# Kernel tuning notes

Hardware: AMD Instinct MI355X
Metric: run time of the kernel (lower is better)

Reference implementation:

```python
import jax, jax.numpy as jnp
import numpy as np

B, SEQ, PRED, ENC = 32, 720, 96, 321
LAYERS, SCALE = 2, 2
SEG = [48, 24]
D = [512, 256]
SNX = [SEQ // s for s in SEG]   # [15, 30]
SNY = [PRED // s for s in SEG]  # [2, 4]


def _gru(x, h, Wih, Whh, bih, bhh):
    # torch.nn.GRUCell math
    gi = x @ Wih.T + bih
    gh = h @ Whh.T + bhh
    i_r, i_z, i_n = jnp.split(gi, 3, axis=-1)
    h_r, h_z, h_n = jnp.split(gh, 3, axis=-1)
    r = jax.nn.sigmoid(i_r + h_r)
    z = jax.nn.sigmoid(i_z + h_z)
    n = jnp.tanh(i_n + r * h_n)
    return (1.0 - z) * n + z * h


def setup_inputs():
    key = jax.random.key(0)
    ks = iter(jax.random.split(key, 40))
    inp = {"x": jax.random.normal(next(ks), (B, SEQ, ENC), jnp.float32)}
    sc = 0.02
    for i in range(LAYERS):
        d, s = D[i], SEG[i]
        inp[f"W_emb{i}"] = jax.random.normal(next(ks), (d, s), jnp.float32) * sc
        inp[f"b_emb{i}"] = jnp.zeros((d,), jnp.float32)
        inp[f"Wih{i}"] = jax.random.normal(next(ks), (3 * d, d), jnp.float32) * sc
        inp[f"Whh{i}"] = jax.random.normal(next(ks), (3 * d, d), jnp.float32) * sc
        inp[f"bih{i}"] = jnp.zeros((3 * d,), jnp.float32)
        inp[f"bhh{i}"] = jnp.zeros((3 * d,), jnp.float32)
        inp[f"Wpred{i}"] = jax.random.normal(next(ks), (s, d), jnp.float32) * sc
        inp[f"bpred{i}"] = jnp.zeros((s,), jnp.float32)
        inp[f"pos{i}"] = jax.random.normal(next(ks), (SNY[i], d // 2), jnp.float32)
        inp[f"chan{i}"] = jax.random.normal(next(ks), (ENC, d // 2), jnp.float32)
    return inp


def _forward(x, params):
    seq_last = jax.lax.stop_gradient(x[:, -1:, :])   # [B,1,ENC] (detached in torch)
    xc = (x - seq_last).transpose(0, 2, 1)            # [B,ENC,SEQ]
    out = jnp.zeros((B, PRED, ENC), x.dtype)
    for i in range(LAYERS):
        p = params[i]
        d, s, T, S = D[i], SEG[i], SNX[i], SNY[i]
        # value embedding: [B*ENC, T, seg_len] -> [B*ENC, T, d]
        xe = jax.nn.relu(jnp.einsum('nts,ds->ntd', xc.reshape(-1, T, s), p['W_emb']) + p['b_emb'])
        if i == 0:
            seq = xe.transpose(1, 0, 2)   # all seg_num_x[0] segments in order
        else:
            # faithful to source: finer layer always consumes segments 0..scale^(i+1)-1
            # once per outer step, seg_num_x[0] times in total
            k = SCALE ** (i + 1)
            idx = np.tile(np.arange(k), SNX[0])
            seq = xe[:, idx].transpose(1, 0, 2)
        h0 = jnp.zeros((xe.shape[0], d), x.dtype)
        step = lambda h, xt: (_gru(xt, h, p['Wih'], p['Whh'], p['bih'], p['bhh']), None)
        h_fin, _ = jax.lax.scan(step, h0, seq)   # [B*ENC, d]
        # decoder: seg_num_y independent GRU cell applications (no carried state)
        half = d // 2
        pos = jnp.concatenate([
            jnp.broadcast_to(p['pos'][None], (ENC, S, half)),
            jnp.broadcast_to(p['chan'][:, None], (ENC, S, half))], axis=-1).reshape(ENC * S, d)
        pos = jnp.tile(pos, (B, 1)).reshape(S, B * ENC, d)   # contiguous chunks per step
        hn = jnp.repeat(h_fin, S, axis=0).reshape(S, B * ENC, d)
        hy = _gru(pos, hn, p['Wih'], p['Whh'], p['bih'], p['bhh'])   # [S, B*ENC, d]
        y = hy.reshape(S * B * ENC, d) @ p['Wpred'].T + p['bpred']   # [S*B*ENC, seg_len]
        y = y.reshape(-1, ENC, PRED).transpose(0, 2, 1)              # [B, PRED, ENC]
        out = out + y + seq_last
    return out / LAYERS


def reference(x, W_emb0, b_emb0, Wih0, Whh0, bih0, bhh0, Wpred0, bpred0, pos0, chan0,
              W_emb1, b_emb1, Wih1, Whh1, bih1, bhh1, Wpred1, bpred1, pos1, chan1):
    params = [
        dict(W_emb=W_emb0, b_emb=b_emb0, Wih=Wih0, Whh=Whh0, bih=bih0, bhh=bhh0,
             Wpred=Wpred0, bpred=bpred0, pos=pos0, chan=chan0),
        dict(W_emb=W_emb1, b_emb=b_emb1, Wih=Wih1, Whh=Whh1, bih=bih1, bhh=bhh1,
             Wpred=Wpred1, bpred=bpred1, pos=pos1, chan=chan1),
    ]
    return _forward(x, params)
```

## Files before the change

### kernel.cpp

```cpp
#include <hip/hip_runtime.h>
#include <math.h>


#define NB     10272
#define MP     10368
#define ENC_   321
#define SEQ_   720
#define PRED_  96
#define BATCH_ 32

typedef long long i64;
typedef unsigned short u16;
typedef unsigned int u32;
using bf16x8 = __attribute__((ext_vector_type(8))) short;
using f32x4  = __attribute__((ext_vector_type(4))) float;
using u16x4  = __attribute__((ext_vector_type(4))) unsigned short;

#define AS1 __attribute__((address_space(1)))
#define AS3 __attribute__((address_space(3)))
#define GLOAD16(g, l) __builtin_amdgcn_global_load_lds((const AS1 void*)(g), (AS3 void*)(l), 16, 0, 0)
#define MFMA16(a, b, c) __builtin_amdgcn_mfma_f32_16x16x32_bf16(a, b, c, 0, 0, 0)

__device__ __forceinline__ float bf2f(u16 u) {
    union { u32 i; float f; } v; v.i = ((u32)u) << 16; return v.f;
}
__device__ __forceinline__ u16 f2bf(float f) {
    union { float f; u32 i; } v; v.f = f;
    return (u16)((v.i + 0x7fff + ((v.i >> 16) & 1)) >> 16);
}
__device__ __forceinline__ float sigf(float x) {
    x = fminf(fmaxf(x, -30.f), 30.f);
    return 1.f / (1.f + __expf(-x));
}
__device__ __forceinline__ float tanhfast(float x) {
    x = fminf(fmaxf(x, -15.f), 15.f);
    float e = __expf(2.f * x);
    return (e - 1.f) / (e + 1.f);
}
__device__ __forceinline__ void swz(int idx, int NXT, int NYT, int& mt, int& nt) {
    int per = NYT * 8;
    int grp = idx / per;
    int base = grp * 8;
    int mg = NXT - base; if (mg > 8) mg = 8;
    int rem = idx - grp * per;
    mt = base + rem % mg;
    nt = rem / mg;
}

__global__ __launch_bounds__(256) void zero_bf(u16* __restrict__ b, i64 n) {
    i64 i = (i64)blockIdx.x * 256 + threadIdx.x;
    i64 n2 = n >> 1;
    if (i < n2) ((u32*)b)[i] = 0;
}

__global__ __launch_bounds__(256) void convert_pad(const float* __restrict__ src,
                                                   u16* __restrict__ dst,
                                                   int R, int C, int Rp, int Cp) {
    i64 idx = (i64)blockIdx.x * 256 + threadIdx.x;
    i64 total = (i64)Rp * Cp;
    if (idx >= total) return;
    int r = (int)(idx / Cp);
    int c = (int)(idx - (i64)r * Cp);
    dst[idx] = (r < R && c < C) ? f2bf(src[(i64)r * C + c]) : (u16)0;
}

__global__ __launch_bounds__(256) void seg_gather_bf(const float* __restrict__ x,
                                                     u16* __restrict__ dst,
                                                     int t0, int T, int s, int Kp) {
    i64 idx = (i64)blockIdx.x * 256 + threadIdx.x;
    i64 per_t = (i64)MP * Kp;
    i64 total = (i64)T * per_t;
    if (idx >= total) return;
    int t = (int)(idx / per_t);
    i64 rem = idx - (i64)t * per_t;
    int j = (int)(rem / MP);
    int n = (int)(rem - (i64)j * MP);
    float v = 0.f;
    if (n < NB && j < s) {
        int b = n / ENC_, e = n - b * ENC_;
        const float* xb = x + (i64)b * SEQ_ * ENC_ + e;
        v = xb[(i64)((t0 + t) * s + j) * ENC_] - xb[(i64)(SEQ_ - 1) * ENC_];
    }
    dst[((i64)t * MP + n) * Kp + j] = f2bf(v);
}

__global__ __launch_bounds__(256) void pmat_fill_bf(const float* __restrict__ pos,
                                                    const float* __restrict__ chan,
                                                    u16* __restrict__ dst,
                                                    int S, int d, int Rp) {
    i64 idx = (i64)blockIdx.x * 256 + threadIdx.x;
    i64 total = (i64)Rp * d;
    if (idx >= total) return;
    int row = (int)(idx / d);
    int c = (int)(idx - (i64)row * d);
    float v = 0.f;
    if (row < ENC_ * S) {
        int e = row / S, sy = row - e * S;
        int half = d >> 1;
        v = (c < half) ? pos[sy * half + c] : chan[e * half + (c - half)];
    }
    dst[idx] = f2bf(v);
}

__global__ __launch_bounds__(256) void out_kernel(const float* __restrict__ x,
                                                  const float* __restrict__ y0,
                                                  const float* __restrict__ y1,
                                                  float* __restrict__ out) {
    int idx = blockIdx.x * 256 + threadIdx.x;
    const int total = BATCH_ * PRED_ * ENC_;
    if (idx >= total) return;
    int b = idx / (PRED_ * ENC_);
    int r = idx - b * (PRED_ * ENC_);
    int p = r / ENC_;
    int e = r - p * ENC_;
    int n = b * ENC_ + e;
    float sl = x[(i64)b * SEQ_ * ENC_ + (i64)(SEQ_ - 1) * ENC_ + e];
    out[idx] = sl + 0.5f * (y0[(i64)n * PRED_ + p] + y1[(i64)n * PRED_ + p]);
}

template<int MODE>
__global__ __launch_bounds__(256) void gemm_bf16mfma(const u16* __restrict__ A,
                                                     const u16* __restrict__ B,
                                                     const float* __restrict__ bias,
                                                     void* __restrict__ Cp,
                                                     int K, int Mstore, int Nstore,
                                                     int ldc, int NXT, int NYT) {
    __shared__ u16 smA[128 * 64];
    __shared__ u16 smB[128 * 64];
    const int tid = threadIdx.x;
    const int w = tid >> 6, l = tid & 63;
    int mt, nt; swz(blockIdx.x, NXT, NYT, mt, nt);
    const int m0 = mt * 128, n0 = nt * 128;
    const int srow = (l >> 3) & 7, pch = l & 7;
    const int cch = pch ^ srow;
    const u16* ga[4]; const u16* gb[4];
#pragma unroll
    for (int r = 0; r < 4; ++r) {
        int seg = r * 4 + w;
        ga[r] = A + (i64)(m0 + seg * 8 + srow) * K + cch * 8;
        gb[r] = B + (i64)(n0 + seg * 8 + srow) * K + cch * 8;
    }
    f32x4 acc[4][4] = {};
    const int lr = l & 15, lg = l >> 4;
    const int wm = (w >> 1) * 64, wn = (w & 1) * 64;
    for (int kk = 0; kk < K; kk += 64) {
#pragma unroll
        for (int r = 0; r < 4; ++r) { GLOAD16(ga[r], smA + (r * 4 + w) * 512); ga[r] += 64; }
#pragma unroll
        for (int r = 0; r < 4; ++r) { GLOAD16(gb[r], smB + (r * 4 + w) * 512); gb[r] += 64; }
        __syncthreads();
#pragma unroll
        for (int s = 0; s < 2; ++s) {
            const int ph = ((s * 4 + lg) ^ (lr & 7)) * 8;
            bf16x8 av[4], bv[4];
#pragma unroll
            for (int i = 0; i < 4; ++i)
                av[i] = *(const bf16x8*)(smA + (wm + i * 16 + lr) * 64 + ph);
#pragma unroll
            for (int j = 0; j < 4; ++j)
                bv[j] = *(const bf16x8*)(smB + (wn + j * 16 + lr) * 64 + ph);
#pragma unroll
            for (int i = 0; i < 4; ++i)
#pragma unroll
                for (int j = 0; j < 4; ++j)
                    acc[i][j] = MFMA16(av[i], bv[j], acc[i][j]);
        }
        __syncthreads();
    }
    if (MODE == 3) {
        const int NCTG = ldc >> 4;
#pragma unroll
        for (int i = 0; i < 4; ++i) {
            int mt16 = (m0 + wm + i * 16) >> 4;
#pragma unroll
            for (int j = 0; j < 4; ++j) {
                int cb = n0 + wn + j * 16;
                if (cb >= Nstore) continue;
                float bs = bias[cb + lr];
                u16x4 sv;
#pragma unroll
                for (int r = 0; r < 4; ++r) sv[r] = f2bf(acc[i][j][r] + bs);
                *(u16x4*)((u16*)Cp + ((i64)mt16 * NCTG + (cb >> 4)) * 256 + l * 4) = sv;
            }
        }
        return;
    }
#pragma unroll
    for (int i = 0; i < 4; ++i) {
        int mbase = m0 + wm + i * 16 + 4 * lg;
#pragma unroll
        for (int j = 0; j < 4; ++j) {
            int c = n0 + wn + j * 16 + lr;
            if (c >= Nstore) continue;
            float bs = bias[c];
#pragma unroll
            for (int r = 0; r < 4; ++r) {
                int mm = mbase + r;
                if (mm < Mstore) {
                    float v = acc[i][j][r] + bs;
                    if (MODE == 2) v = fmaxf(v, 0.f);
                    if (MODE == 0) ((float*)Cp)[(i64)mm * ldc + c] = v;
                    else           ((u16*)Cp)[(i64)mm * ldc + c] = f2bf(v);
                }
            }
        }
    }
}

template<int D>
__global__ __launch_bounds__(256, 3) void gru_step(const u16* __restrict__ xe,
                                                   const u16* __restrict__ hsrc,
                                                   const u16* __restrict__ Wih,
                                                   const u16* __restrict__ Whh,
                                                   const float* __restrict__ bih,
                                                   const float* __restrict__ bhh,
                                                   u16* __restrict__ hdst) {
    __shared__ u16 smA[64 * 64];
    __shared__ u16 smB[3 * 64 * 64];
    __shared__ u16 smH[64 * 64];
    const int tid = threadIdx.x;
    const int w = tid >> 6, l = tid & 63;
    const int m0 = blockIdx.x * 64;
    const int c0 = blockIdx.y * 64;
    const int srow = (l >> 3) & 7, pch = l & 7;
    const int cch = pch ^ srow;
    const int lr = l & 15, lg = l >> 4;
    f32x4 aR[4] = {}, aZ[4] = {}, aNI[4] = {}, aNH[4] = {};
#pragma unroll
    for (int phase = 0; phase < 2; ++phase) {
        const u16* Abase = phase ? hsrc : xe;
        const u16* Bbase = phase ? Whh : Wih;
        const u16* ga[2]; const u16* gb[6];
#pragma unroll
        for (int r = 0; r < 2; ++r)
            ga[r] = Abase + (i64)(m0 + (r * 4 + w) * 8 + srow) * D + cch * 8;
#pragma unroll
        for (int q = 0; q < 6; ++q) {
            int gs = q * 4 + w;
            int g = gs >> 3, sp = gs & 7;
            gb[q] = Bbase + (i64)(g * D + c0 + sp * 8 + srow) * D + cch * 8;
        }
        for (int kk = 0; kk < D; kk += 64) {
#pragma unroll
            for (int r = 0; r < 2; ++r) GLOAD16(ga[r], smA + (r * 4 + w) * 512);
            if (phase == 1 && kk == c0) {
#pragma unroll
                for (int r = 0; r < 2; ++r) GLOAD16(ga[r], smH + (r * 4 + w) * 512);
            }
#pragma unroll
            for (int r = 0; r < 2; ++r) ga[r] += 64;
#pragma unroll
            for (int q = 0; q < 6; ++q) { GLOAD16(gb[q], smB + (q * 4 + w) * 512); gb[q] += 64; }
            __syncthreads();
#pragma unroll
            for (int s = 0; s < 2; ++s) {
                const int phs = ((s * 4 + lg) ^ (lr & 7)) * 8;
                bf16x8 av = *(const bf16x8*)(smA + (w * 16 + lr) * 64 + phs);
#pragma unroll
                for (int j = 0; j < 4; ++j) {
                    bf16x8 b0 = *(const bf16x8*)(smB + 0 * 4096 + (j * 16 + lr) * 64 + phs);
                    bf16x8 b1 = *(const bf16x8*)(smB + 1 * 4096 + (j * 16 + lr) * 64 + phs);
                    bf16x8 b2 = *(const bf16x8*)(smB + 2 * 4096 + (j * 16 + lr) * 64 + phs);
                    aR[j] = MFMA16(av, b0, aR[j]);
                    aZ[j] = MFMA16(av, b1, aZ[j]);
                    if (phase == 0)
                        aNI[j] = MFMA16(av, b2, aNI[j]);
                    else
                        aNH[j] = MFMA16(av, b2, aNH[j]);
                }
            }
            __syncthreads();
        }
    }
    const int rowb = m0 + w * 16 + 4 * lg;
#pragma unroll
    for (int j = 0; j < 4; ++j) {
        const int cc = c0 + j * 16 + lr;
        float bR = bih[cc] + bhh[cc];
        float bZ = bih[D + cc] + bhh[D + cc];
        float bNI = bih[2 * D + cc];
        float bNH = bhh[2 * D + cc];
#pragma unroll
        for (int r = 0; r < 4; ++r) {
            const int lrow = w * 16 + 4 * lg + r;
            const int lcol = j * 16 + lr;
            float ho = bf2f(smH[lrow * 64 + ((((lcol >> 3)) ^ (lrow & 7)) << 3) + (lcol & 7)]);
            float rr = sigf(aR[j][r] + bR);
            float zz = sigf(aZ[j][r] + bZ);
            float nn = tanhfast(aNI[j][r] + bNI + rr * (aNH[j][r] + bNH));
            hdst[(i64)(rowb + r) * D + cc] = f2bf((1.f - zz) * nn + zz * ho);
        }
    }
}

template<int D>
__global__ __launch_bounds__(256, 3) void gru_step_h(const u16* __restrict__ gi,
                                                     const u16* __restrict__ hsrc,
                                                     const u16* __restrict__ Whh,
                                                     const float* __restrict__ bhh,
                                                     u16* __restrict__ hdst) {
    constexpr int NCT = D / 16;
    constexpr int NCTG = 3 * D / 16;
    __shared__ u16 smA[64 * 64];
    __shared__ u16 smB[3 * 64 * 64];
    __shared__ u16 smH[64 * 64];
    const int tid = threadIdx.x;
    const int w = tid >> 6, l = tid & 63;
    const int m0 = blockIdx.x * 64;
    const int c0 = blockIdx.y * 64;
    const int srow = (l >> 3) & 7, pch = l & 7;
    const int cch = pch ^ srow;
    const int lr = l & 15, lg = l >> 4;
    f32x4 aR[4] = {}, aZ[4] = {}, aNH[4] = {};
    const u16* ga[2]; const u16* gb[6];
#pragma unroll
    for (int r = 0; r < 2; ++r)
        ga[r] = hsrc + (i64)(m0 + (r * 4 + w) * 8 + srow) * D + cch * 8;
#pragma unroll
    for (int q = 0; q < 6; ++q) {
        int gs = q * 4 + w;
        int g = gs >> 3, sp = gs & 7;
        gb[q] = Whh + (i64)(g * D + c0 + sp * 8 + srow) * D + cch * 8;
    }
    const int Trow = (m0 >> 4) + w;
    const i64 gbase = (i64)Trow * NCTG * 256 + l * 4;
    u16x4 g0[4], g1[4], g2[4];
    for (int kk = 0; kk < D; kk += 64) {
#pragma unroll
        for (int r = 0; r < 2; ++r) GLOAD16(ga[r], smA + (r * 4 + w) * 512);
        if (kk == c0) {
#pragma unroll
            for (int r = 0; r < 2; ++r) GLOAD16(ga[r], smH + (r * 4 + w) * 512);
        }
#pragma unroll
        for (int r = 0; r < 2; ++r) ga[r] += 64;
#pragma unroll
        for (int q = 0; q < 6; ++q) { GLOAD16(gb[q], smB + (q * 4 + w) * 512); gb[q] += 64; }
        __syncthreads();
        if (kk == D - 64) {
#pragma unroll
            for (int j = 0; j < 4; ++j) {
                const int ct = (c0 >> 4) + j;
                g0[j] = *(const u16x4*)(gi + gbase + (i64)(0 * NCT + ct) * 256);
                g1[j] = *(const u16x4*)(gi + gbase + (i64)(1 * NCT + ct) * 256);
                g2[j] = *(const u16x4*)(gi + gbase + (i64)(2 * NCT + ct) * 256);
            }
        }
#pragma unroll
        for (int s = 0; s < 2; ++s) {
            const int phs = ((s * 4 + lg) ^ (lr & 7)) * 8;
            bf16x8 av = *(const bf16x8*)(smA + (w * 16 + lr) * 64 + phs);
#pragma unroll
            for (int j = 0; j < 4; ++j) {
                bf16x8 b0 = *(const bf16x8*)(smB + 0 * 4096 + (j * 16 + lr) * 64 + phs);
                bf16x8 b1 = *(const bf16x8*)(smB + 1 * 4096 + (j * 16 + lr) * 64 + phs);
                bf16x8 b2 = *(const bf16x8*)(smB + 2 * 4096 + (j * 16 + lr) * 64 + phs);
                aR[j] = MFMA16(av, b0, aR[j]);
                aZ[j] = MFMA16(av, b1, aZ[j]);
                aNH[j] = MFMA16(av, b2, aNH[j]);
            }
        }
        __syncthreads();
    }
    const int rowb = m0 + w * 16 + 4 * lg;
#pragma unroll
    for (int j = 0; j < 4; ++j) {
        const int cc = c0 + j * 16 + lr;
        float bR = bhh[cc];
        float bZ = bhh[D + cc];
        float bNH = bhh[2 * D + cc];
#pragma unroll
        for (int r = 0; r < 4; ++r) {
            const int lrow = w * 16 + 4 * lg + r;
            const int lcol = j * 16 + lr;
            float ho = bf2f(smH[lrow * 64 + ((((lcol >> 3)) ^ (lrow & 7)) << 3) + (lcol & 7)]);
            float rr = sigf(bf2f(g0[j][r]) + aR[j][r] + bR);
            float zz = sigf(bf2f(g1[j][r]) + aZ[j][r] + bZ);
            float nn = tanhfast(bf2f(g2[j][r]) + rr * (aNH[j][r] + bNH));
            hdst[(i64)(rowb + r) * D + cc] = f2bf((1.f - zz) * nn + zz * ho);
        }
    }
}

template<int D, int S>
__global__ __launch_bounds__(256) void gru_dec(const u16* __restrict__ Asrc,
                                               const u16* __restrict__ Whh,
                                               const float* __restrict__ bhh,
                                               const u16* __restrict__ gi,
                                               u16* __restrict__ hy) {
    constexpr int NYT = D / 64;
    __shared__ u16 smA[128 * 64];
    __shared__ u16 smB[3 * 64 * 64];
    const int tid = threadIdx.x;
    const int w = tid >> 6, l = tid & 63;
    int mt, nt; swz(blockIdx.x, 81, NYT, mt, nt);
    const int m0 = mt * 128;
    const int c0 = nt * 64;
    const int srow = (l >> 3) & 7, pch = l & 7;
    const int cch = pch ^ srow;
    const u16* ga[4]; const u16* gb[6];
#pragma unroll
    for (int r = 0; r < 4; ++r)
        ga[r] = Asrc + (i64)(m0 + (r * 4 + w) * 8 + srow) * D + cch * 8;
#pragma unroll
    for (int q = 0; q < 6; ++q) {
        int gs = q * 4 + w;
        int g = gs >> 3, sp = gs & 7;
        gb[q] = Whh + (i64)(g * D + c0 + sp * 8 + srow) * D + cch * 8;
    }
    f32x4 acc[3][4][2] = {};
    const int lr = l & 15, lg = l >> 4;
    const int wm = (w >> 1) * 64, wc = (w & 1) * 32;
    for (int kk = 0; kk < D; kk += 64) {
#pragma unroll
        for (int r = 0; r < 4; ++r) { GLOAD16(ga[r], smA + (r * 4 + w) * 512); ga[r] += 64; }
#pragma unroll
        for (int q = 0; q < 6; ++q) { GLOAD16(gb[q], smB + (q * 4 + w) * 512); gb[q] += 64; }
        __syncthreads();
#pragma unroll
        for (int s = 0; s < 2; ++s) {
            const int ph = ((s * 4 + lg) ^ (lr & 7)) * 8;
            bf16x8 av[4], bv[3][2];
#pragma unroll
            for (int i = 0; i < 4; ++i)
                av[i] = *(const bf16x8*)(smA + (wm + i * 16 + lr) * 64 + ph);
#pragma unroll
            for (int g = 0; g < 3; ++g)
#pragma unroll
                for (int j = 0; j < 2; ++j)
                    bv[g][j] = *(const bf16x8*)(smB + g * 4096 + (wc + j * 16 + lr) * 64 + ph);
#pragma unroll
            for (int g = 0; g < 3; ++g)
#pragma unroll
                for (int i = 0; i < 4; ++i)
#pragma unroll
                    for (int j = 0; j < 2; ++j)
                        acc[g][i][j] = MFMA16(av[i], bv[g][j], acc[g][i][j]);
        }
        __syncthreads();
    }
#pragma unroll
    for (int i = 0; i < 4; ++i) {
        const int rowb = m0 + wm + 16 * i + 4 * lg;
        int e0 = rowb % ENC_;
#pragma unroll
        for (int j = 0; j < 2; ++j) {
            const int cc = c0 + wc + 16 * j + lr;
            float b0 = bhh[cc], b1 = bhh[D + cc], b2 = bhh[2 * D + cc];
#pragma unroll
            for (int r = 0; r < 4; ++r) {
                int mm = rowb + r;
                if (mm >= NB) continue;
                int e = e0 + r; if (e >= ENC_) e -= ENC_;
                float ho = bf2f(Asrc[(i64)mm * D + cc]);
                float hr = acc[0][i][j][r] + b0;
                float hz = acc[1][i][j][r] + b1;
                float hn2 = acc[2][i][j][r] + b2;
#pragma unroll
                for (int sy = 0; sy < S; ++sy) {
                    i64 gib = (i64)(e * S + sy) * 3 * D + cc;
                    float rr = sigf(bf2f(gi[gib]) + hr);
                    float zz = sigf(bf2f(gi[gib + D]) + hz);
                    float nn = tanhfast(bf2f(gi[gib + 2 * D]) + rr * hn2);
                    hy[((i64)mm * S + sy) * D + cc] = f2bf((1.f - zz) * nn + zz * ho);
                }
            }
        }
    }
}

extern "C" void kernel_launch(void* const* d_in, const int* in_sizes, int n_in,
                              void* d_out, int out_size, void* d_ws, size_t ws_size,
                              hipStream_t stream) {
    const float* x      = (const float*)d_in[0];
    const float* W_emb0 = (const float*)d_in[1];
    const float* b_emb0 = (const float*)d_in[2];
    const float* Wih0   = (const float*)d_in[3];
    const float* Whh0   = (const float*)d_in[4];
    const float* bih0   = (const float*)d_in[5];
    const float* bhh0   = (const float*)d_in[6];
    const float* Wpred0 = (const float*)d_in[7];
    const float* bpred0 = (const float*)d_in[8];
    const float* pos0   = (const float*)d_in[9];
    const float* chan0  = (const float*)d_in[10];
    const float* W_emb1 = (const float*)d_in[11];
    const float* b_emb1 = (const float*)d_in[12];
    const float* Wih1   = (const float*)d_in[13];
    const float* Whh1   = (const float*)d_in[14];
    const float* bih1   = (const float*)d_in[15];
    const float* bhh1   = (const float*)d_in[16];
    const float* Wpred1 = (const float*)d_in[17];
    const float* bpred1 = (const float*)d_in[18];
    const float* pos1   = (const float*)d_in[19];
    const float* chan1  = (const float*)d_in[20];
    float* out = (float*)d_out;

    i64 off = 0;
    char* base = (char*)d_ws;
    auto alloc = [&](i64 bytes) -> void* {
        void* p = base + off; off += (bytes + 255) & ~(i64)255; return p;
    };
    u16*   f_mirA  = (u16*)  alloc((i64)MP * 512 * 2);
    u16*   f_mirB  = (u16*)  alloc((i64)MP * 512 * 2);
    u16*   wih0b   = (u16*)  alloc((i64)1536 * 512 * 2);
    u16*   whh0b   = (u16*)  alloc((i64)1536 * 512 * 2);
    u16*   wih1b   = (u16*)  alloc((i64)768 * 256 * 2);
    u16*   whh1b   = (u16*)  alloc((i64)768 * 256 * 2);
    u16*   we0b    = (u16*)  alloc((i64)512 * 64 * 2);
    u16*   we1b    = (u16*)  alloc((i64)256 * 64 * 2);
    u16*   wp0b    = (u16*)  alloc((i64)128 * 512 * 2);
    u16*   wp1b    = (u16*)  alloc((i64)128 * 256 * 2);
    u16*   f_pm0   = (u16*)  alloc((i64)768 * 512 * 2);
    u16*   f_pm1   = (u16*)  alloc((i64)1408 * 256 * 2);
    u16*   f_gidec = (u16*)  alloc((i64)768 * 1536 * 2);
    u16*   f_hy    = (u16*)  alloc((i64)4 * NB * 256 * 2);
    float* f_y0    = (float*)alloc((i64)NB * 96 * 4);
    float* f_y1    = (float*)alloc((i64)NB * 96 * 4);
    i64 fixed = off;

    char* R = base + fixed;
    i64 a1 = (((i64)4 * MP * 64 * 2) + 255) & ~(i64)255;
    i64 a2 = (((i64)4 * MP * 256 * 2) + 255) & ~(i64)255;
    i64 a3 = (i64)4 * MP * 768 * 2;
    i64 R1 = a1 + a2 + a3;
    u16* f_seg1 = (u16*)R;
    u16* f_xe1  = (u16*)(R + a1);
    u16* f_gi1  = (u16*)(R + a1 + a2);
    int gsz = 1;
    {
        const int cand[4] = {15, 5, 3, 2};
        for (int ii = 0; ii < 4; ++ii) {
            i64 need = (i64)cand[ii] * MP * (64 + 512) * 2 + 2 * 256;
            i64 tot = fixed + (need > R1 ? need : R1);
            if (tot <= (i64)ws_size) { gsz = cand[ii]; break; }
        }
    }
    u16* f_seg0 = (u16*)R;
    i64 s1 = (((i64)gsz * MP * 64 * 2) + 255) & ~(i64)255;
    u16* f_xe0 = (u16*)(R + s1);

    auto cvt = [&](const float* s, u16* dst, int Rr, int C, int Rp, int Cp) {
        i64 tot = (i64)Rp * Cp;
        convert_pad<<<(int)((tot + 255) / 256), 256, 0, stream>>>(s, dst, Rr, C, Rp, Cp);
    };
    auto gemmN = [&](const u16* A, const u16* B, const float* bias, void* C,
                     int gx, int Nc, int K, int Mstore, int ldc, int mode) {
        int NYT = (Nc + 127) / 128;
        dim3 g(gx * NYT);
        if (mode == 0)      gemm_bf16mfma<0><<<g, 256, 0, stream>>>(A, B, bias, C, K, Mstore, Nc, ldc, gx, NYT);
        else if (mode == 1) gemm_bf16mfma<1><<<g, 256, 0, stream>>>(A, B, bias, C, K, Mstore, Nc, ldc, gx, NYT);
        else if (mode == 2) gemm_bf16mfma<2><<<g, 256, 0, stream>>>(A, B, bias, C, K, Mstore, Nc, ldc, gx, NYT);
        else                gemm_bf16mfma<3><<<g, 256, 0, stream>>>(A, B, bias, C, K, Mstore, Nc, ldc, gx, NYT);
    };

    cvt(Wih0, wih0b, 1536, 512, 1536, 512);
    cvt(Whh0, whh0b, 1536, 512, 1536, 512);
    cvt(Wih1, wih1b, 768, 256, 768, 256);
    cvt(Whh1, whh1b, 768, 256, 768, 256);
    cvt(W_emb0, we0b, 512, 48, 512, 64);
    cvt(W_emb1, we1b, 256, 24, 256, 64);
    cvt(Wpred0, wp0b, 48, 512, 128, 512);
    cvt(Wpred1, wp1b, 24, 256, 128, 256);
    pmat_fill_bf<<<(int)(((i64)768 * 512 + 255) / 256), 256, 0, stream>>>(pos0, chan0, f_pm0, 2, 512, 768);
    pmat_fill_bf<<<(int)(((i64)1408 * 256 + 255) / 256), 256, 0, stream>>>(pos1, chan1, f_pm1, 4, 256, 1408);

    {
        i64 n = (i64)MP * 512;
        zero_bf<<<(int)((n / 2 + 255) / 256), 256, 0, stream>>>(f_mirA, n);
    }
    for (int t0 = 0; t0 < 15;) {
        int g = 15 - t0 < gsz ? 15 - t0 : gsz;
        i64 tot = (i64)g * MP * 64;
        seg_gather_bf<<<(int)((tot + 255) / 256), 256, 0, stream>>>(x, f_seg0, t0, g, 48, 64);
        gemmN(f_seg0, we0b, b_emb0, f_xe0, g * 81, 512, 64, g * MP, 512, 2);
        for (int s = 0; s < g; ++s) {
            int tg = t0 + s;
            const u16* Asrc = (tg & 1) ? f_mirB : f_mirA;
            u16* Adst = (tg & 1) ? f_mirA : f_mirB;
            gru_step<512><<<dim3(162, 8), 256, 0, stream>>>(
                f_xe0 + (i64)s * MP * 512, Asrc, wih0b, whh0b, bih0, bhh0, Adst);
        }
        t0 += g;
    }
    gemmN(f_pm0, wih0b, bih0, f_gidec, 6, 1536, 512, 642, 1536, 1);
    gru_dec<512, 2><<<dim3(81 * 8), 256, 0, stream>>>(
        f_mirB, whh0b, bhh0, f_gidec, f_hy);
    gemmN(f_hy, wp0b, bpred0, f_y0, 161, 48, 512, 2 * NB, 48, 0);

    {
        i64 n = (i64)MP * 256;
        zero_bf<<<(int)((n / 2 + 255) / 256), 256, 0, stream>>>(f_mirA, n);
    }
    {
        i64 tot = (i64)4 * MP * 64;
        seg_gather_bf<<<(int)((tot + 255) / 256), 256, 0, stream>>>(x, f_seg1, 0, 4, 24, 64);
    }
    gemmN(f_seg1, we1b, b_emb1, f_xe1, 324, 256, 64, 4 * MP, 256, 2);
    gemmN(f_xe1, wih1b, bih1, f_gi1, 324, 768, 256, 4 * MP, 768, 3);
    for (int t = 0; t < 60; ++t) {
        const u16* Asrc = (t & 1) ? f_mirB : f_mirA;
        u16* Adst = (t & 1) ? f_mirA : f_mirB;
        gru_step_h<256><<<dim3(162, 4), 256, 0, stream>>>(
            f_gi1 + (i64)(t & 3) * MP * 768, Asrc, whh1b, bhh1, Adst);
    }
    gemmN(f_pm1, wih1b, bih1, f_gidec, 11, 768, 256, 1284, 768, 1);
    gru_dec<256, 4><<<dim3(81 * 4), 256, 0, stream>>>(
        f_mirA, whh1b, bhh1, f_gidec, f_hy);
    gemmN(f_hy, wp1b, bpred1, f_y1, 321, 24, 256, 4 * NB, 24, 0);

    out_kernel<<<(BATCH_ * PRED_ * ENC_ + 255) / 256, 256, 0, stream>>>(x, f_y0, f_y1, out);
}
```

Measured before the change: 2.174 ms.

## Precompute layer-0 input-gate GEMM in bulk and use hidden-only GRU step

Layer 0 now computes the input projections for a whole group of timesteps with one large batched GEMM (mode 3) and then runs the recurrent gru_step_h kernel, which only multiplies by Whh. This replaces the fused kernel that did both the Wih and Whh GEMMs inside every sequential step. It moves half the per-step MFMA work into a large, more parallel GEMM off the recurrence's critical path. In exchange it needs extra workspace to store the precomputed gates, which lowers the timestep group size to at most 5, and the gates make a round trip through memory in bf16.

```diff
diff --git a/kernel.cpp b/kernel.cpp
--- a/kernel.cpp
+++ b/kernel.cpp
@@ -203,92 +203,6 @@
                     else           ((u16*)Cp)[(i64)mm * ldc + c] = f2bf(v);
                 }
             }
-        }
-    }
-}
-
-template<int D>
-__global__ __launch_bounds__(256, 3) void gru_step(const u16* __restrict__ xe,
-                                                   const u16* __restrict__ hsrc,
-                                                   const u16* __restrict__ Wih,
-                                                   const u16* __restrict__ Whh,
-                                                   const float* __restrict__ bih,
-                                                   const float* __restrict__ bhh,
-                                                   u16* __restrict__ hdst) {
-    __shared__ u16 smA[64 * 64];
-    __shared__ u16 smB[3 * 64 * 64];
-    __shared__ u16 smH[64 * 64];
-    const int tid = threadIdx.x;
-    const int w = tid >> 6, l = tid & 63;
-    const int m0 = blockIdx.x * 64;
-    const int c0 = blockIdx.y * 64;
-    const int srow = (l >> 3) & 7, pch = l & 7;
-    const int cch = pch ^ srow;
-    const int lr = l & 15, lg = l >> 4;
-    f32x4 aR[4] = {}, aZ[4] = {}, aNI[4] = {}, aNH[4] = {};
-#pragma unroll
-    for (int phase = 0; phase < 2; ++phase) {
-        const u16* Abase = phase ? hsrc : xe;
-        const u16* Bbase = phase ? Whh : Wih;
-        const u16* ga[2]; const u16* gb[6];
-#pragma unroll
-        for (int r = 0; r < 2; ++r)
-            ga[r] = Abase + (i64)(m0 + (r * 4 + w) * 8 + srow) * D + cch * 8;
-#pragma unroll
-        for (int q = 0; q < 6; ++q) {
-            int gs = q * 4 + w;
-            int g = gs >> 3, sp = gs & 7;
-            gb[q] = Bbase + (i64)(g * D + c0 + sp * 8 + srow) * D + cch * 8;
-        }
-        for (int kk = 0; kk < D; kk += 64) {
-#pragma unroll
-            for (int r = 0; r < 2; ++r) GLOAD16(ga[r], smA + (r * 4 + w) * 512);
-            if (phase == 1 && kk == c0) {
-#pragma unroll
-                for (int r = 0; r < 2; ++r) GLOAD16(ga[r], smH + (r * 4 + w) * 512);
-            }
-#pragma unroll
-            for (int r = 0; r < 2; ++r) ga[r] += 64;
-#pragma unroll
-            for (int q = 0; q < 6; ++q) { GLOAD16(gb[q], smB + (q * 4 + w) * 512); gb[q] += 64; }
-            __syncthreads();
-#pragma unroll
-            for (int s = 0; s < 2; ++s) {
-                const int phs = ((s * 4 + lg) ^ (lr & 7)) * 8;
-                bf16x8 av = *(const bf16x8*)(smA + (w * 16 + lr) * 64 + phs);
-#pragma unroll
-                for (int j = 0; j < 4; ++j) {
-                    bf16x8 b0 = *(const bf16x8*)(smB + 0 * 4096 + (j * 16 + lr) * 64 + phs);
-                    bf16x8 b1 = *(const bf16x8*)(smB + 1 * 4096 + (j * 16 + lr) * 64 + phs);
-                    bf16x8 b2 = *(const bf16x8*)(smB + 2 * 4096 + (j * 16 + lr) * 64 + phs);
-                    aR[j] = MFMA16(av, b0, aR[j]);
-                    aZ[j] = MFMA16(av, b1, aZ[j]);
-                    if (phase == 0)
-                        aNI[j] = MFMA16(av, b2, aNI[j]);
-                    else
-                        aNH[j] = MFMA16(av, b2, aNH[j]);
-                }
-            }
-            __syncthreads();
-        }
-    }
-    const int rowb = m0 + w * 16 + 4 * lg;
-#pragma unroll
-    for (int j = 0; j < 4; ++j) {
-        const int cc = c0 + j * 16 + lr;
-        float bR = bih[cc] + bhh[cc];
-        float bZ = bih[D + cc] + bhh[D + cc];
-        float bNI = bih[2 * D + cc];
-        float bNH = bhh[2 * D + cc];
-#pragma unroll
-        for (int r = 0; r < 4; ++r) {
-            const int lrow = w * 16 + 4 * lg + r;
-            const int lcol = j * 16 + lr;
-            float ho = bf2f(smH[lrow * 64 + ((((lcol >> 3)) ^ (lrow & 7)) << 3) + (lcol & 7)]);
-            float rr = sigf(aR[j][r] + bR);
-            float zz = sigf(aZ[j][r] + bZ);
-            float nn = tanhfast(aNI[j][r] + bNI + rr * (aNH[j][r] + bNH));
-            hdst[(i64)(rowb + r) * D + cc] = f2bf((1.f - zz) * nn + zz * ho);
         }
     }
 }
@@ -528,16 +442,18 @@
     u16* f_gi1  = (u16*)(R + a1 + a2);
     int gsz = 1;
     {
-        const int cand[4] = {15, 5, 3, 2};
+        const int cand[4] = {5, 3, 2, 1};
         for (int ii = 0; ii < 4; ++ii) {
-            i64 need = (i64)cand[ii] * MP * (64 + 512) * 2 + 2 * 256;
+            i64 need = (i64)cand[ii] * MP * (64 + 512 + 1536) * 2 + 3 * 256;
             i64 tot = fixed + (need > R1 ? need : R1);
             if (tot <= (i64)ws_size) { gsz = cand[ii]; break; }
         }
     }
     u16* f_seg0 = (u16*)R;
-    i64 s1 = (((i64)gsz * MP * 64 * 2) + 255) & ~(i64)255;
-    u16* f_xe0 = (u16*)(R + s1);
+    i64 s0a = (((i64)gsz * MP * 64 * 2) + 255) & ~(i64)255;
+    i64 s0b = (((i64)gsz * MP * 512 * 2) + 255) & ~(i64)255;
+    u16* f_xe0 = (u16*)(R + s0a);
+    u16* f_gi0 = (u16*)(R + s0a + s0b);
 
     auto cvt = [&](const float* s, u16* dst, int Rr, int C, int Rp, int Cp) {
         i64 tot = (i64)Rp * Cp;
@@ -573,12 +489,13 @@
         i64 tot = (i64)g * MP * 64;
         seg_gather_bf<<<(int)((tot + 255) / 256), 256, 0, stream>>>(x, f_seg0, t0, g, 48, 64);
         gemmN(f_seg0, we0b, b_emb0, f_xe0, g * 81, 512, 64, g * MP, 512, 2);
+        gemmN(f_xe0, wih0b, bih0, f_gi0, g * 81, 1536, 512, g * MP, 1536, 3);
         for (int s = 0; s < g; ++s) {
             int tg = t0 + s;
             const u16* Asrc = (tg & 1) ? f_mirB : f_mirA;
             u16* Adst = (tg & 1) ? f_mirA : f_mirB;
-            gru_step<512><<<dim3(162, 8), 256, 0, stream>>>(
-                f_xe0 + (i64)s * MP * 512, Asrc, wih0b, whh0b, bih0, bhh0, Adst);
+            gru_step_h<512><<<dim3(162, 8), 256, 0, stream>>>(
+                f_gi0 + (i64)s * MP * 1536, Asrc, whh0b, bhh0, Adst);
         }
         t0 += g;
     }
```

Result: slower. 2.396 ms (+10.2%).

## Co-schedule layer0 and layer1 GRU recurrences in one combined kernel launch

Applied to the files above, without the earlier changes.

Layer 0 and layer 1 GRU recurrences are independent, so the first 15 steps of layer 1 now run in the same launch as the 15 layer-0 steps, with blockIdx.y choosing which layer a block computes. The layer-1 embedding and input-gate GEMMs are moved ahead of the layer-0 loop, and layer 1 gets its own hidden-state ping-pong buffers and a fixed gi1 allocation. This removes 15 separate small launches and fills the GPU better during the layer-0 steps. In exchange, fixed workspace use grows and a smaller gsz may be chosen for layer 0.

```diff
diff --git a/kernel.cpp b/kernel.cpp
--- a/kernel.cpp
+++ b/kernel.cpp
@@ -208,20 +208,19 @@
 }
 
 template<int D>
-__global__ __launch_bounds__(256, 3) void gru_step(const u16* __restrict__ xe,
-                                                   const u16* __restrict__ hsrc,
-                                                   const u16* __restrict__ Wih,
-                                                   const u16* __restrict__ Whh,
-                                                   const float* __restrict__ bih,
-                                                   const float* __restrict__ bhh,
-                                                   u16* __restrict__ hdst) {
-    __shared__ u16 smA[64 * 64];
-    __shared__ u16 smB[3 * 64 * 64];
-    __shared__ u16 smH[64 * 64];
+__device__ __forceinline__ void gru_step_body(const u16* __restrict__ xe,
+                                              const u16* __restrict__ hsrc,
+                                              const u16* __restrict__ Wih,
+                                              const u16* __restrict__ Whh,
+                                              const float* __restrict__ bih,
+                                              const float* __restrict__ bhh,
+                                              u16* __restrict__ hdst,
+                                              int bx, int by,
+                                              u16* smA, u16* smB, u16* smH) {
     const int tid = threadIdx.x;
     const int w = tid >> 6, l = tid & 63;
-    const int m0 = blockIdx.x * 64;
-    const int c0 = blockIdx.y * 64;
+    const int m0 = bx * 64;
+    const int c0 = by * 64;
     const int srow = (l >> 3) & 7, pch = l & 7;
     const int cch = pch ^ srow;
     const int lr = l & 15, lg = l >> 4;
@@ -294,20 +293,19 @@
 }
 
 template<int D>
-__global__ __launch_bounds__(256, 3) void gru_step_h(const u16* __restrict__ gi,
-                                                     const u16* __restrict__ hsrc,
-                                                     const u16* __restrict__ Whh,
-                                                     const float* __restrict__ bhh,
-                                                     u16* __restrict__ hdst) {
+__device__ __forceinline__ void gru_step_h_body(const u16* __restrict__ gi,
+                                                const u16* __restrict__ hsrc,
+                                                const u16* __restrict__ Whh,
+                                                const float* __restrict__ bhh,
+                                                u16* __restrict__ hdst,
+                                                int bx, int by,
+                                                u16* smA, u16* smB, u16* smH) {
     constexpr int NCT = D / 16;
     constexpr int NCTG = 3 * D / 16;
-    __shared__ u16 smA[64 * 64];
-    __shared__ u16 smB[3 * 64 * 64];
-    __shared__ u16 smH[64 * 64];
     const int tid = threadIdx.x;
     const int w = tid >> 6, l = tid & 63;
-    const int m0 = blockIdx.x * 64;
-    const int c0 = blockIdx.y * 64;
+    const int m0 = bx * 64;
+    const int c0 = by * 64;
     const int srow = (l >> 3) & 7, pch = l & 7;
     const int cch = pch ^ srow;
     const int lr = l & 15, lg = l >> 4;
@@ -380,6 +378,37 @@
             hdst[(i64)(rowb + r) * D + cc] = f2bf((1.f - zz) * nn + zz * ho);
         }
     }
+}
+
+template<int D>
+__global__ __launch_bounds__(256, 3) void gru_step_h(const u16* __restrict__ gi,
+                                                     const u16* __restrict__ hsrc,
+                                                     const u16* __restrict__ Whh,
+                                                     const float* __restrict__ bhh,
+                                                     u16* __restrict__ hdst) {
+    __shared__ u16 smA[64 * 64];
+    __shared__ u16 smB[3 * 64 * 64];
+    __shared__ u16 smH[64 * 64];
+    gru_step_h_body<D>(gi, hsrc, Whh, bhh, hdst, blockIdx.x, blockIdx.y, smA, smB, smH);
+}
+
+__global__ __launch_bounds__(256, 3) void gru_step_comb(
+    const u16* __restrict__ xe0, const u16* __restrict__ h0src,
+    const u16* __restrict__ Wih0, const u16* __restrict__ Whh0,
+    const float* __restrict__ bih0, const float* __restrict__ bhh0,
+    u16* __restrict__ h0dst,
+    const u16* __restrict__ gi1, const u16* __restrict__ h1src,
+    const u16* __restrict__ Whh1, const float* __restrict__ bhh1,
+    u16* __restrict__ h1dst) {
+    __shared__ u16 smA[64 * 64];
+    __shared__ u16 smB[3 * 64 * 64];
+    __shared__ u16 smH[64 * 64];
+    if (blockIdx.y < 8)
+        gru_step_body<512>(xe0, h0src, Wih0, Whh0, bih0, bhh0, h0dst,
+                           blockIdx.x, blockIdx.y, smA, smB, smH);
+    else
+        gru_step_h_body<256>(gi1, h1src, Whh1, bhh1, h1dst,
+                             blockIdx.x, blockIdx.y - 8, smA, smB, smH);
 }
 
 template<int D, int S>
@@ -502,6 +531,8 @@
     };
     u16*   f_mirA  = (u16*)  alloc((i64)MP * 512 * 2);
     u16*   f_mirB  = (u16*)  alloc((i64)MP * 512 * 2);
+    u16*   f_m1A   = (u16*)  alloc((i64)MP * 256 * 2);
+    u16*   f_m1B   = (u16*)  alloc((i64)MP * 256 * 2);
     u16*   wih0b   = (u16*)  alloc((i64)1536 * 512 * 2);
     u16*   whh0b   = (u16*)  alloc((i64)1536 * 512 * 2);
     u16*   wih1b   = (u16*)  alloc((i64)768 * 256 * 2);
@@ -516,16 +547,15 @@
     u16*   f_hy    = (u16*)  alloc((i64)4 * NB * 256 * 2);
     float* f_y0    = (float*)alloc((i64)NB * 96 * 4);
     float* f_y1    = (float*)alloc((i64)NB * 96 * 4);
+    u16*   f_gi1   = (u16*)  alloc((i64)4 * MP * 768 * 2);
     i64 fixed = off;
 
     char* R = base + fixed;
     i64 a1 = (((i64)4 * MP * 64 * 2) + 255) & ~(i64)255;
-    i64 a2 = (((i64)4 * MP * 256 * 2) + 255) & ~(i64)255;
-    i64 a3 = (i64)4 * MP * 768 * 2;
-    i64 R1 = a1 + a2 + a3;
+    i64 a2 = (i64)4 * MP * 256 * 2;
+    i64 R1 = a1 + a2;
     u16* f_seg1 = (u16*)R;
     u16* f_xe1  = (u16*)(R + a1);
-    u16* f_gi1  = (u16*)(R + a1 + a2);
     int gsz = 1;
     {
         const int cand[4] = {15, 5, 3, 2};
@@ -565,9 +595,16 @@
     pmat_fill_bf<<<(int)(((i64)1408 * 256 + 255) / 256), 256, 0, stream>>>(pos1, chan1, f_pm1, 4, 256, 1408);
 
     {
-        i64 n = (i64)MP * 512;
-        zero_bf<<<(int)((n / 2 + 255) / 256), 256, 0, stream>>>(f_mirA, n);
-    }
+        i64 n0 = (i64)MP * 512;
+        zero_bf<<<(int)((n0 / 2 + 255) / 256), 256, 0, stream>>>(f_mirA, n0);
+        i64 n1 = (i64)MP * 256;
+        zero_bf<<<(int)((n1 / 2 + 255) / 256), 256, 0, stream>>>(f_m1A, n1);
+        i64 tot = (i64)4 * MP * 64;
+        seg_gather_bf<<<(int)((tot + 255) / 256), 256, 0, stream>>>(x, f_seg1, 0, 4, 24, 64);
+    }
+    gemmN(f_seg1, we1b, b_emb1, f_xe1, 324, 256, 64, 4 * MP, 256, 2);
+    gemmN(f_xe1, wih1b, bih1, f_gi1, 324, 768, 256, 4 * MP, 768, 3);
+
     for (int t0 = 0; t0 < 15;) {
         int g = 15 - t0 < gsz ? 15 - t0 : gsz;
         i64 tot = (i64)g * MP * 64;
@@ -575,37 +612,31 @@
         gemmN(f_seg0, we0b, b_emb0, f_xe0, g * 81, 512, 64, g * MP, 512, 2);
         for (int s = 0; s < g; ++s) {
             int tg = t0 + s;
-            const u16* Asrc = (tg & 1) ? f_mirB : f_mirA;
-            u16* Adst = (tg & 1) ? f_mirA : f_mirB;
-            gru_step<512><<<dim3(162, 8), 256, 0, stream>>>(
-                f_xe0 + (i64)s * MP * 512, Asrc, wih0b, whh0b, bih0, bhh0, Adst);
+            const u16* A0s = (tg & 1) ? f_mirB : f_mirA;
+            u16* A0d = (tg & 1) ? f_mirA : f_mirB;
+            const u16* A1s = (tg & 1) ? f_m1B : f_m1A;
+            u16* A1d = (tg & 1) ? f_m1A : f_m1B;
+            gru_step_comb<<<dim3(162, 12), 256, 0, stream>>>(
+                f_xe0 + (i64)s * MP * 512, A0s, wih0b, whh0b, bih0, bhh0, A0d,
+                f_gi1 + (i64)(tg & 3) * MP * 768, A1s, whh1b, bhh1, A1d);
         }
         t0 += g;
     }
+    for (int t = 15; t < 60; ++t) {
+        const u16* A1s = (t & 1) ? f_m1B : f_m1A;
+        u16* A1d = (t & 1) ? f_m1A : f_m1B;
+        gru_step_h<256><<<dim3(162, 4), 256, 0, stream>>>(
+            f_gi1 + (i64)(t & 3) * MP * 768, A1s, whh1b, bhh1, A1d);
+    }
+
     gemmN(f_pm0, wih0b, bih0, f_gidec, 6, 1536, 512, 642, 1536, 1);
     gru_dec<512, 2><<<dim3(81 * 8), 256, 0, stream>>>(
         f_mirB, whh0b, bhh0, f_gidec, f_hy);
     gemmN(f_hy, wp0b, bpred0, f_y0, 161, 48, 512, 2 * NB, 48, 0);
 
-    {
-        i64 n = (i64)MP * 256;
-        zero_bf<<<(int)((n / 2 + 255) / 256), 256, 0, stream>>>(f_mirA, n);
-    }
-    {
-        i64 tot = (i64)4 * MP * 64;
-        seg_gather_bf<<<(int)((tot + 255) / 256), 256, 0, stream>>>(x, f_seg1, 0, 4, 24, 64);
-    }
-    gemmN(f_seg1, we1b, b_emb1, f_xe1, 324, 256, 64, 4 * MP, 256, 2);
-    gemmN(f_xe1, wih1b, bih1, f_gi1, 324, 768, 256, 4 * MP, 768, 3);
-    for (int t = 0; t < 60; ++t) {
-        const u16* Asrc = (t & 1) ? f_mirB : f_mirA;
-        u16* Adst = (t & 1) ? f_mirA : f_mirB;
-        gru_step_h<256><<<dim3(162, 4), 256, 0, stream>>>(
-            f_gi1 + (i64)(t & 3) * MP * 768, Asrc, whh1b, bhh1, Adst);
-    }
     gemmN(f_pm1, wih1b, bih1, f_gidec, 11, 768, 256, 1284, 768, 1);
     gru_dec<256, 4><<<dim3(81 * 4), 256, 0, stream>>>(
-        f_mirA, whh1b, bhh1, f_gidec, f_hy);
+        f_m1A, whh1b, bhh1, f_gidec, f_hy);
     gemmN(f_hy, wp1b, bpred1, f_y1, 321, 24, 256, 4 * NB, 24, 0);
 
     out_kernel<<<(BATCH_ * PRED_ * ENC_ + 255) / 256, 256, 0, stream>>>(x, f_y0, f_y1, out);
```

After: 2.016 ms. 7.3% less time.
